# Performance work log

Hardware: AMD Instinct MI355X
Metric: run time of the kernel (lower is better)

Reference implementation:

```python
import jax, jax.numpy as jnp
import numpy as np

N, B, H, C, NF = 200000, 100, 128, 3, 128


def setup_inputs() -> dict:
    key = jax.random.key(0)
    ks = jax.random.split(key, 12)
    def w(k, shape, s=0.05):
        return jax.random.normal(k, shape, jnp.float32) * s
    return dict(
        node_feat=w(ks[0], (N, NF), 1.0),
        coord=w(ks[1], (N, 3), 1.0),
        virtual_node_feat=w(ks[2], (B, NF, C), 1.0),
        virtual_coord=w(ks[3], (B, 3, C), 1.0),
        data_batch=jnp.sort(jax.random.randint(ks[4], (N,), 0, B)),
        We1=w(ks[5], (2 * NF + 1, H)), be1=jnp.zeros((H,), jnp.float32),
        We2=w(ks[6], (H, H)), be2=jnp.zeros((H,), jnp.float32),
        Wc1=w(ks[7], (H, H)), bc1=jnp.zeros((H,), jnp.float32),
        Wc2=w(ks[8], (H, 1), 0.001),  # xavier gain=0.001 layer, no bias
        Wn1=w(ks[9], (2 * H, H)), bn1=jnp.zeros((H,), jnp.float32),
        Wn2=w(ks[10], (H, H)), bn2=jnp.zeros((H,), jnp.float32),
    )


def _segment_mean(x, idx, num_segments):
    # x: [N, d1, d2] -> [num_segments, d1, d2]; mean over nodes of each graph
    sums = jax.ops.segment_sum(x, idx, num_segments=num_segments)
    counts = jax.ops.segment_sum(jnp.ones((x.shape[0],), x.dtype), idx,
                                 num_segments=num_segments)
    return sums / jnp.maximum(counts, 1.0)[:, None, None]


def reference(node_feat, coord, virtual_node_feat, virtual_coord, data_batch,
              We1, be1, We2, be2, Wc1, bc1, Wc2, Wn1, bn1, Wn2, bn2):
    silu = jax.nn.silu
    n, nf = node_feat.shape
    nb, _, c = virtual_coord.shape

    # gather: real node -> its graph's virtual nodes
    diff = virtual_coord[data_batch] - coord[:, :, None]            # [N,3,C]
    radial = jnp.linalg.norm(diff, axis=1)                          # [N,C]

    # edge model (work in [N,C,feat] layout to avoid permutes)
    feat_R = jnp.broadcast_to(node_feat[:, None, :], (n, c, nf))    # [N,C,NF]
    feat_V = virtual_node_feat[data_batch].transpose(0, 2, 1)       # [N,C,NF]
    e_in = jnp.concatenate([feat_R, feat_V, radial[:, :, None]], axis=-1)
    m = silu(e_in @ We1 + be1)
    m = silu(m @ We2 + be2)                                         # [N,C,H]

    # coord model: per (node, virtual-channel) scalar weight
    s = silu(m @ Wc1 + bc1) @ Wc2                                   # [N,C,1]
    trans = diff * s[:, :, 0][:, None, :]                           # [N,3,C]
    virtual_coord = virtual_coord + _segment_mean(trans, data_batch, nb)

    # node model on virtual nodes
    agg = _segment_mean(m, data_batch, nb)                          # [B,C,H]
    n_in = jnp.concatenate([virtual_node_feat.transpose(0, 2, 1), agg], axis=-1)
    h = silu(n_in @ Wn1 + bn1) @ Wn2 + bn2                          # [B,C,H]
    virtual_node_feat = virtual_node_feat + h.transpose(0, 2, 1)    # residual

    return virtual_node_feat, virtual_coord
```

## Files before the change

kernel.cpp:

```cpp
#include <hip/hip_runtime.h>
#include <hip/hip_bf16.h>
#include <math.h>

#define NNODES 200000
#define NGRAPH 100
#define HD     128
#define NCH    3
#define BN     64
#define EROWS  (BN*NCH)
#define ESTR   136

typedef short short8 __attribute__((ext_vector_type(8)));
typedef float f32x4  __attribute__((ext_vector_type(4)));

#define MFMA_16x16x32(a,b,c) __builtin_amdgcn_mfma_f32_16x16x32_bf16((a),(b),(c),0,0,0)

__device__ __forceinline__ float bf2f(unsigned short u) {
    return __uint_as_float(((unsigned int)u) << 16);
}
__device__ __forceinline__ unsigned short f2bf(float f) {
    return (unsigned short)((__float_as_uint(f) + 0x8000u) >> 16);
}
__device__ __forceinline__ float silu_f(float x) {
    return x * __builtin_amdgcn_rcpf(1.0f + __expf(-x));
}

__global__ void prep_kernel(const float* __restrict__ We1,
                            const float* __restrict__ We2,
                            const float* __restrict__ Wc1,
                            const float* __restrict__ be1,
                            const float* __restrict__ be2,
                            const float* __restrict__ bc1,
                            const float* __restrict__ Wc2,
                            const float* __restrict__ vnf,
                            unsigned short* __restrict__ w1r,
                            unsigned short* __restrict__ w2r,
                            unsigned short* __restrict__ wc1r,
                            float* __restrict__ Q,
                            float* __restrict__ wlast,
                            float* __restrict__ be1f,
                            float* __restrict__ be2f,
                            float* __restrict__ bc1f,
                            float* __restrict__ wc2f) {
    int bid = blockIdx.x;
    if (bid < 192) {
        int t = bid * 256 + threadIdx.x;
        int m  = t / 16384;
        int e  = t % 16384;
        int j  = e & 7;
        int l  = (e >> 3) & 63;
        int ks = (e >> 9) & 3;
        int ct = e >> 11;
        int row = ks * 32 + (l >> 4) * 8 + j;
        int col = ct * 16 + (l & 15);
        const float*    src = (m == 0) ? We1 : ((m == 1) ? We2 : Wc1);
        unsigned short* dst = (m == 0) ? w1r : ((m == 1) ? w2r : wc1r);
        dst[e] = f2bf(src[row * 128 + col]);
        if (t < 128) {
            wlast[t] = We1[256 * 128 + t];
            be1f[t]  = be1[t];
            be2f[t]  = be2[t];
            bc1f[t]  = bc1[t];
            wc2f[t]  = Wc2[t];
        }
    } else {
        int bc = bid - 192;
        int b = bc / NCH, c = bc % NCH;
        int t = threadIdx.x;
        __shared__ float v[128];
        if (t < 128) v[t] = vnf[(b * 128 + t) * 3 + c];
        __syncthreads();
        if (t < 128) {
            float s = 0.0f;
            for (int k = 0; k < 128; ++k)
                s += v[k] * We1[(128 + k) * 128 + t];
            Q[(b * 3 + c) * 128 + t] = s;
        }
    }
}

__global__ __launch_bounds__(256, 2) void egcl_main(
    const float* __restrict__ node_feat,
    const float* __restrict__ coord,
    const float* __restrict__ vcoord,
    const int*   __restrict__ batch,
    const unsigned short* __restrict__ w1r,
    const unsigned short* __restrict__ w2r,
    const unsigned short* __restrict__ wc1r,
    const float* __restrict__ Q,
    const float* __restrict__ wlast,
    const float* __restrict__ be1f,
    const float* __restrict__ be2f,
    const float* __restrict__ bc1f,
    const float* __restrict__ wc2f,
    float* __restrict__ aggsum,
    float* __restrict__ transsum,
    float* __restrict__ cnt)
{
    __shared__ __align__(16) unsigned short e_buf[EROWS * ESTR];
    __shared__ unsigned short sbatch[BN];
    __shared__ unsigned short sseg_start[BN + 1];
    __shared__ unsigned short sseg_b[BN];
    __shared__ int snseg;

    const int tid   = threadIdx.x;
    const int wave  = tid >> 6;
    const int lane  = tid & 63;
    const int lrow  = lane & 15;
    const int lkb   = (lane >> 4) * 8;
    const int rq    = (lane >> 4) * 4;
    const int node0 = blockIdx.x * BN;

    if (tid < BN) {
        int n = node0 + tid;
        int b = batch[n];
        sbatch[tid] = (unsigned short)b;
        int prev = (tid > 0) ? batch[n - 1] : -1;
        unsigned long long mask = __ballot(b != prev);
        int ns = __popcll(mask);
        if (b != prev) {
            int idx = __popcll(mask & ((1ull << tid) - 1ull));
            sseg_start[idx] = (unsigned short)tid;
            sseg_b[idx]     = (unsigned short)b;
        }
        if (tid == 0) { sseg_start[ns] = BN; snseg = ns; }
        float cx = coord[n * 3 + 0];
        float cy = coord[n * 3 + 1];
        float cz = coord[n * 3 + 2];
        for (int c = 0; c < 3; ++c) {
            float dx = vcoord[b * 9 + 0 * 3 + c] - cx;
            float dy = vcoord[b * 9 + 1 * 3 + c] - cy;
            float dz = vcoord[b * 9 + 2 * 3 + c] - cz;
            f32x4 pad;
            pad[0] = dx; pad[1] = dy; pad[2] = dz;
            pad[3] = sqrtf(dx * dx + dy * dy + dz * dz);
            *(f32x4*)&e_buf[(c * 64 + tid) * ESTR + 128] = pad;
        }
    }
    __syncthreads();
    const int nseg = snseg;

    f32x4 acc1[8] = {};
    {
        const float* arow = node_feat + (size_t)(node0 + wave * 16 + lrow) * 128;
        for (int ks = 0; ks < 4; ++ks) {
            f32x4 x0 = *(const f32x4*)(arow + ks * 32 + lkb);
            f32x4 x1 = *(const f32x4*)(arow + ks * 32 + lkb + 4);
            short8 af;
            af[0] = (short)f2bf(x0[0]); af[1] = (short)f2bf(x0[1]);
            af[2] = (short)f2bf(x0[2]); af[3] = (short)f2bf(x0[3]);
            af[4] = (short)f2bf(x1[0]); af[5] = (short)f2bf(x1[1]);
            af[6] = (short)f2bf(x1[2]); af[7] = (short)f2bf(x1[3]);
            for (int ct = 0; ct < 8; ++ct) {
                short8 bfg = *(const short8*)(w1r + ((ct * 4 + ks) * 64 + lane) * 8);
                acc1[ct] = MFMA_16x16x32(af, bfg, acc1[ct]);
            }
        }
    }
    {
        float wl[8], bb[8];
        #pragma unroll
        for (int ct = 0; ct < 8; ++ct) {
            wl[ct] = wlast[ct * 16 + lrow];
            bb[ct] = be1f[ct * 16 + lrow];
        }
        if (nseg == 1) {
            const float* qb = Q + (int)sseg_b[0] * (NCH * HD);
            float qv[3][8];
            #pragma unroll
            for (int c = 0; c < 3; ++c)
                #pragma unroll
                for (int ct = 0; ct < 8; ++ct)
                    qv[c][ct] = qb[c * 128 + ct * 16 + lrow];
            #pragma unroll
            for (int r = 0; r < 4; ++r) {
                int nl = wave * 16 + rq + r;
                #pragma unroll
                for (int c = 0; c < 3; ++c) {
                    int row = c * 64 + nl;
                    float rad = *(const float*)&e_buf[row * ESTR + 134];
                    #pragma unroll
                    for (int ct = 0; ct < 8; ++ct) {
                        float x = acc1[ct][r] + bb[ct] + qv[c][ct] + rad * wl[ct];
                        e_buf[row * ESTR + ct * 16 + lrow] = f2bf(silu_f(x));
                    }
                }
            }
        } else {
            #pragma unroll
            for (int r = 0; r < 4; ++r) {
                int nl = wave * 16 + rq + r;
                int b  = sbatch[nl];
                #pragma unroll
                for (int c = 0; c < 3; ++c) {
                    int row = c * 64 + nl;
                    float rad = *(const float*)&e_buf[row * ESTR + 134];
                    const float* qb = Q + (b * 3 + c) * 128;
                    #pragma unroll
                    for (int ct = 0; ct < 8; ++ct) {
                        float x = acc1[ct][r] + bb[ct] + qb[ct * 16 + lrow] + rad * wl[ct];
                        e_buf[row * ESTR + ct * 16 + lrow] = f2bf(silu_f(x));
                    }
                }
            }
        }
    }

    const int bagg = (nseg == 1) ? (int)sseg_b[0] * (NCH * HD) : 0;

    for (int half = 0; half < 2; ++half) {
        f32x4 acc[3][4] = {};
        for (int ks = 0; ks < 4; ++ks) {
            short8 af[3];
            #pragma unroll
            for (int j = 0; j < 3; ++j)
                af[j] = *(const short8*)(&e_buf[(j * 64 + wave * 16 + lrow) * ESTR +
                                                ks * 32 + lkb]);
            #pragma unroll
            for (int c4 = 0; c4 < 4; ++c4) {
                int ct = half * 4 + c4;
                short8 bfg = *(const short8*)(w2r + ((ct * 4 + ks) * 64 + lane) * 8);
                #pragma unroll
                for (int j = 0; j < 3; ++j)
                    acc[j][c4] = MFMA_16x16x32(af[j], bfg, acc[j][c4]);
            }
        }
        for (int j = 0; j < 3; ++j) {
            #pragma unroll
            for (int c4 = 0; c4 < 4; ++c4) {
                int ct = half * 4 + c4;
                int h = ct * 16 + lrow;
                float bb = be2f[h];
                float psum = 0.0f;
                #pragma unroll
                for (int r = 0; r < 4; ++r) {
                    int row = j * 64 + wave * 16 + rq + r;
                    float v = silu_f(acc[j][c4][r] + bb);
                    e_buf[row * ESTR + h] = f2bf(v);
                    psum += v;
                }
                if (nseg == 1) {
                    psum += __shfl_xor(psum, 16, 64);
                    psum += __shfl_xor(psum, 32, 64);
                    if (lane < 16)
                        atomicAdd(&aggsum[bagg + j * 128 + ct * 16 + lane], psum);
                }
            }
        }
    }

    float p[3][4] = {};
    for (int half = 0; half < 2; ++half) {
        f32x4 acc[3][4] = {};
        for (int ks = 0; ks < 4; ++ks) {
            short8 af[3];
            #pragma unroll
            for (int j = 0; j < 3; ++j)
                af[j] = *(const short8*)(&e_buf[(j * 64 + wave * 16 + lrow) * ESTR +
                                                ks * 32 + lkb]);
            #pragma unroll
            for (int c4 = 0; c4 < 4; ++c4) {
                int ct = half * 4 + c4;
                short8 bfg = *(const short8*)(wc1r + ((ct * 4 + ks) * 64 + lane) * 8);
                #pragma unroll
                for (int j = 0; j < 3; ++j)
                    acc[j][c4] = MFMA_16x16x32(af[j], bfg, acc[j][c4]);
            }
        }
        for (int j = 0; j < 3; ++j) {
            #pragma unroll
            for (int c4 = 0; c4 < 4; ++c4) {
                int ct = half * 4 + c4;
                int h = ct * 16 + lrow;
                float bb = bc1f[h];
                float w2 = wc2f[h];
                #pragma unroll
                for (int r = 0; r < 4; ++r)
                    p[j][r] += silu_f(acc[j][c4][r] + bb) * w2;
            }
        }
    }
    for (int j = 0; j < 3; ++j) {
        float p0 = p[j][0], p1 = p[j][1], p2 = p[j][2], p3 = p[j][3];
        #pragma unroll
        for (int off = 1; off < 16; off <<= 1) {
            p0 += __shfl_xor(p0, off, 64);
            p1 += __shfl_xor(p1, off, 64);
            p2 += __shfl_xor(p2, off, 64);
            p3 += __shfl_xor(p3, off, 64);
        }
        if (lrow == 0) {
            int rbase = j * 64 + wave * 16 + rq;
            *(float*)&e_buf[(rbase + 0) * ESTR + 134] = p0;
            *(float*)&e_buf[(rbase + 1) * ESTR + 134] = p1;
            *(float*)&e_buf[(rbase + 2) * ESTR + 134] = p2;
            *(float*)&e_buf[(rbase + 3) * ESTR + 134] = p3;
        }
    }
    __syncthreads();

    if (nseg == 1) {
        int b = sseg_b[0];
        if (wave == 0) {
            float t[9];
            #pragma unroll
            for (int c = 0; c < 3; ++c) {
                int row = c * 64 + lane;
                float sv = *(const float*)&e_buf[row * ESTR + 134];
                float dx = *(const float*)&e_buf[row * ESTR + 128];
                float dy = *(const float*)&e_buf[row * ESTR + 130];
                float dz = *(const float*)&e_buf[row * ESTR + 132];
                t[0 * 3 + c] = dx * sv;
                t[1 * 3 + c] = dy * sv;
                t[2 * 3 + c] = dz * sv;
            }
            #pragma unroll
            for (int off = 1; off < 64; off <<= 1)
                #pragma unroll
                for (int k = 0; k < 9; ++k)
                    t[k] += __shfl_xor(t[k], off, 64);
            if (lane < 9)
                atomicAdd(&transsum[b * 9 + lane],
                          __shfl(t[lane], 0, 64));
            if (lane == 0) atomicAdd(&cnt[b], 64.0f);
        }
    } else {
        for (int sg = 0; sg < nseg; ++sg) {
            int s0 = sseg_start[sg], s1 = sseg_start[sg + 1], b = sseg_b[sg];
            for (int idx = tid; idx < NCH * HD; idx += 256) {
                int c = idx >> 7, h = idx & 127;
                float sum = 0.f;
                for (int ii = s0; ii < s1; ++ii)
                    sum += bf2f(e_buf[(c * 64 + ii) * ESTR + h]);
                atomicAdd(&aggsum[(b * 3 + c) * 128 + h], sum);
            }
            if (tid < 9) {
                int d = tid / 3, c = tid % 3;
                float sum = 0.f;
                for (int ii = s0; ii < s1; ++ii)
                    sum += (*(const float*)&e_buf[(c * 64 + ii) * ESTR + 128 + 2 * d])
                           * (*(const float*)&e_buf[(c * 64 + ii) * ESTR + 134]);
                atomicAdd(&transsum[b * 9 + d * 3 + c], sum);
            }
            if (tid == 0) atomicAdd(&cnt[b], (float)(s1 - s0));
        }
    }
}

__global__ void finalize_kernel(const float* __restrict__ vnf,
                                const float* __restrict__ vcoord,
                                const float* __restrict__ Wn1,
                                const float* __restrict__ bn1,
                                const float* __restrict__ Wn2,
                                const float* __restrict__ bn2,
                                const float* __restrict__ aggsum,
                                const float* __restrict__ transsum,
                                const float* __restrict__ cnt,
                                float* __restrict__ out) {
    int b = blockIdx.x / NCH;
    int c = blockIdx.x % NCH;
    int j = threadIdx.x;
    __shared__ float nin[256];
    __shared__ float h1[128];
    float count = fmaxf(cnt[b], 1.0f);
    nin[j]       = vnf[(b * 128 + j) * 3 + c];
    nin[128 + j] = aggsum[(b * 3 + c) * 128 + j] / count;
    __syncthreads();
    float x = bn1[j];
    for (int k = 0; k < 256; ++k)
        x += nin[k] * Wn1[k * 128 + j];
    h1[j] = silu_f(x);
    __syncthreads();
    float y = bn2[j];
    for (int k = 0; k < 128; ++k)
        y += h1[k] * Wn2[k * 128 + j];
    out[(b * 128 + j) * 3 + c] = vnf[(b * 128 + j) * 3 + c] + y;
    if (c == 0 && j < 9) {
        out[NGRAPH * 128 * 3 + b * 9 + j] =
            vcoord[b * 9 + j] + transsum[b * 9 + j] / count;
    }
}

extern "C" void kernel_launch(void* const* d_in, const int* in_sizes, int n_in,
                              void* d_out, int out_size, void* d_ws, size_t ws_size,
                              hipStream_t stream) {
    const float* node_feat = (const float*)d_in[0];
    const float* coord     = (const float*)d_in[1];
    const float* vnf       = (const float*)d_in[2];
    const float* vcoord    = (const float*)d_in[3];
    const int*   batch     = (const int*)d_in[4];
    const float* We1 = (const float*)d_in[5];
    const float* be1 = (const float*)d_in[6];
    const float* We2 = (const float*)d_in[7];
    const float* be2 = (const float*)d_in[8];
    const float* Wc1 = (const float*)d_in[9];
    const float* bc1 = (const float*)d_in[10];
    const float* Wc2 = (const float*)d_in[11];
    const float* Wn1 = (const float*)d_in[12];
    const float* bn1 = (const float*)d_in[13];
    const float* Wn2 = (const float*)d_in[14];
    const float* bn2 = (const float*)d_in[15];

    char* ws = (char*)d_ws;
    float*          aggsum   = (float*)(ws + 0);
    float*          transsum = (float*)(ws + 153600);
    float*          cntp     = (float*)(ws + 157200);
    float*          Q        = (float*)(ws + 157600);
    unsigned short* w1r      = (unsigned short*)(ws + 311200);
    unsigned short* w2r      = (unsigned short*)(ws + 343968);
    unsigned short* wc1r     = (unsigned short*)(ws + 376736);
    float*          wlast    = (float*)(ws + 409504);
    float*          be1f     = (float*)(ws + 410016);
    float*          be2f     = (float*)(ws + 410528);
    float*          bc1f     = (float*)(ws + 411040);
    float*          wc2f     = (float*)(ws + 411552);

    (void)hipMemsetAsync(d_ws, 0, 157600, stream);

    prep_kernel<<<192 + NGRAPH * NCH, 256, 0, stream>>>(
        We1, We2, Wc1, be1, be2, bc1, Wc2, vnf,
        w1r, w2r, wc1r, Q, wlast, be1f, be2f, bc1f, wc2f);

    egcl_main<<<NNODES / BN, 256, 0, stream>>>(
        node_feat, coord, vcoord, batch, w1r, w2r, wc1r, Q,
        wlast, be1f, be2f, bc1f, wc2f, aggsum, transsum, cntp);

    finalize_kernel<<<NGRAPH * NCH, 128, 0, stream>>>(
        vnf, vcoord, Wn1, bn1, Wn2, bn2, aggsum, transsum, cntp,
        (float*)d_out);
}
```

Measured before the change: 323.0 us.

## Permute hidden layout for vectorized bf16 LDS stores, packed converts, fold memset into prep

```diff
diff --git a/kernel.cpp b/kernel.cpp
--- a/kernel.cpp
+++ b/kernel.cpp
@@ -12,6 +12,8 @@
 
 typedef short short8 __attribute__((ext_vector_type(8)));
 typedef float f32x4  __attribute__((ext_vector_type(4)));
+typedef unsigned int u32x2 __attribute__((ext_vector_type(2)));
+typedef unsigned int u32x4 __attribute__((ext_vector_type(4)));
 
 #define MFMA_16x16x32(a,b,c) __builtin_amdgcn_mfma_f32_16x16x32_bf16((a),(b),(c),0,0,0)
 
@@ -20,6 +22,14 @@
 }
 __device__ __forceinline__ unsigned short f2bf(float f) {
     return (unsigned short)((__float_as_uint(f) + 0x8000u) >> 16);
+}
+__device__ __forceinline__ unsigned int cvt_pk_bf16(float lo, float hi) {
+    unsigned int r;
+    asm("v_cvt_pk_bf16_f32 %0, %1, %2" : "=v"(r) : "v"(lo), "v"(hi));
+    return r;
+}
+__device__ __forceinline__ short8 as_short8(u32x4 v) {
+    union { u32x4 u; short8 s; } x; x.u = v; return x.s;
 }
 __device__ __forceinline__ float silu_f(float x) {
     return x * __builtin_amdgcn_rcpf(1.0f + __expf(-x));
@@ -41,7 +51,8 @@
                             float* __restrict__ be1f,
                             float* __restrict__ be2f,
                             float* __restrict__ bc1f,
-                            float* __restrict__ wc2f) {
+                            float* __restrict__ wc2f,
+                            float* __restrict__ zacc) {
     int bid = blockIdx.x;
     if (bid < 192) {
         int t = bid * 256 + threadIdx.x;
@@ -51,11 +62,12 @@
         int l  = (e >> 3) & 63;
         int ks = (e >> 9) & 3;
         int ct = e >> 11;
-        int row = ks * 32 + (l >> 4) * 8 + j;
+        int kf  = ks * 32 + (l >> 4) * 8 + j;
         int col = ct * 16 + (l & 15);
+        int srck = (m == 0) ? kf : (((kf & 7) << 4) | (kf >> 3));
         const float*    src = (m == 0) ? We1 : ((m == 1) ? We2 : Wc1);
         unsigned short* dst = (m == 0) ? w1r : ((m == 1) ? w2r : wc1r);
-        dst[e] = f2bf(src[row * 128 + col]);
+        dst[e] = f2bf(src[srck * 128 + col]);
         if (t < 128) {
             wlast[t] = We1[256 * 128 + t];
             be1f[t]  = be1[t];
@@ -63,7 +75,7 @@
             bc1f[t]  = bc1[t];
             wc2f[t]  = Wc2[t];
         }
-    } else {
+    } else if (bid < 492) {
         int bc = bid - 192;
         int b = bc / NCH, c = bc % NCH;
         int t = threadIdx.x;
@@ -76,6 +88,9 @@
                 s += v[k] * We1[(128 + k) * 128 + t];
             Q[(b * 3 + c) * 128 + t] = s;
         }
+    } else {
+        int idx = (bid - 492) * 256 + threadIdx.x;
+        if (idx < 39400) zacc[idx] = 0.0f;
     }
 }
 
@@ -146,11 +161,12 @@
         for (int ks = 0; ks < 4; ++ks) {
             f32x4 x0 = *(const f32x4*)(arow + ks * 32 + lkb);
             f32x4 x1 = *(const f32x4*)(arow + ks * 32 + lkb + 4);
-            short8 af;
-            af[0] = (short)f2bf(x0[0]); af[1] = (short)f2bf(x0[1]);
-            af[2] = (short)f2bf(x0[2]); af[3] = (short)f2bf(x0[3]);
-            af[4] = (short)f2bf(x1[0]); af[5] = (short)f2bf(x1[1]);
-            af[6] = (short)f2bf(x1[2]); af[7] = (short)f2bf(x1[3]);
+            u32x4 av;
+            av[0] = cvt_pk_bf16(x0[0], x0[1]);
+            av[1] = cvt_pk_bf16(x0[2], x0[3]);
+            av[2] = cvt_pk_bf16(x1[0], x1[1]);
+            av[3] = cvt_pk_bf16(x1[2], x1[3]);
+            short8 af = as_short8(av);
             for (int ct = 0; ct < 8; ++ct) {
                 short8 bfg = *(const short8*)(w1r + ((ct * 4 + ks) * 64 + lane) * 8);
                 acc1[ct] = MFMA_16x16x32(af, bfg, acc1[ct]);
@@ -158,12 +174,10 @@
         }
     }
     {
-        float wl[8], bb[8];
+        float wl[8];
         #pragma unroll
-        for (int ct = 0; ct < 8; ++ct) {
+        for (int ct = 0; ct < 8; ++ct)
             wl[ct] = wlast[ct * 16 + lrow];
-            bb[ct] = be1f[ct * 16 + lrow];
-        }
         if (nseg == 1) {
             const float* qb = Q + (int)sseg_b[0] * (NCH * HD);
             float qv[3][8];
@@ -171,7 +185,7 @@
             for (int c = 0; c < 3; ++c)
                 #pragma unroll
                 for (int ct = 0; ct < 8; ++ct)
-                    qv[c][ct] = qb[c * 128 + ct * 16 + lrow];
+                    qv[c][ct] = qb[c * 128 + ct * 16 + lrow] + be1f[ct * 16 + lrow];
             #pragma unroll
             for (int r = 0; r < 4; ++r) {
                 int nl = wave * 16 + rq + r;
@@ -179,14 +193,23 @@
                 for (int c = 0; c < 3; ++c) {
                     int row = c * 64 + nl;
                     float rad = *(const float*)&e_buf[row * ESTR + 134];
+                    float v[8];
                     #pragma unroll
-                    for (int ct = 0; ct < 8; ++ct) {
-                        float x = acc1[ct][r] + bb[ct] + qv[c][ct] + rad * wl[ct];
-                        e_buf[row * ESTR + ct * 16 + lrow] = f2bf(silu_f(x));
-                    }
+                    for (int ct = 0; ct < 8; ++ct)
+                        v[ct] = silu_f(acc1[ct][r] + qv[c][ct] + rad * wl[ct]);
+                    u32x4 av;
+                    av[0] = cvt_pk_bf16(v[0], v[1]);
+                    av[1] = cvt_pk_bf16(v[2], v[3]);
+                    av[2] = cvt_pk_bf16(v[4], v[5]);
+                    av[3] = cvt_pk_bf16(v[6], v[7]);
+                    *(u32x4*)&e_buf[row * ESTR + lrow * 8] = av;
                 }
             }
         } else {
+            float bb[8];
+            #pragma unroll
+            for (int ct = 0; ct < 8; ++ct)
+                bb[ct] = be1f[ct * 16 + lrow];
             #pragma unroll
             for (int r = 0; r < 4; ++r) {
                 int nl = wave * 16 + rq + r;
@@ -196,11 +219,17 @@
                     int row = c * 64 + nl;
                     float rad = *(const float*)&e_buf[row * ESTR + 134];
                     const float* qb = Q + (b * 3 + c) * 128;
+                    float v[8];
                     #pragma unroll
-                    for (int ct = 0; ct < 8; ++ct) {
-                        float x = acc1[ct][r] + bb[ct] + qb[ct * 16 + lrow] + rad * wl[ct];
-                        e_buf[row * ESTR + ct * 16 + lrow] = f2bf(silu_f(x));
-                    }
+                    for (int ct = 0; ct < 8; ++ct)
+                        v[ct] = silu_f(acc1[ct][r] + bb[ct] + qb[ct * 16 + lrow]
+                                       + rad * wl[ct]);
+                    u32x4 av;
+                    av[0] = cvt_pk_bf16(v[0], v[1]);
+                    av[1] = cvt_pk_bf16(v[2], v[3]);
+                    av[2] = cvt_pk_bf16(v[4], v[5]);
+                    av[3] = cvt_pk_bf16(v[6], v[7]);
+                    *(u32x4*)&e_buf[row * ESTR + lrow * 8] = av;
                 }
             }
         }
@@ -225,25 +254,36 @@
                     acc[j][c4] = MFMA_16x16x32(af[j], bfg, acc[j][c4]);
             }
         }
+        float b0 = be2f[(half * 4 + 0) * 16 + lrow];
+        float b1 = be2f[(half * 4 + 1) * 16 + lrow];
+        float b2 = be2f[(half * 4 + 2) * 16 + lrow];
+        float b3 = be2f[(half * 4 + 3) * 16 + lrow];
+        #pragma unroll
         for (int j = 0; j < 3; ++j) {
-            #pragma unroll
-            for (int c4 = 0; c4 < 4; ++c4) {
-                int ct = half * 4 + c4;
-                int h = ct * 16 + lrow;
-                float bb = be2f[h];
-                float psum = 0.0f;
-                #pragma unroll
-                for (int r = 0; r < 4; ++r) {
-                    int row = j * 64 + wave * 16 + rq + r;
-                    float v = silu_f(acc[j][c4][r] + bb);
-                    e_buf[row * ESTR + h] = f2bf(v);
-                    psum += v;
-                }
-                if (nseg == 1) {
-                    psum += __shfl_xor(psum, 16, 64);
-                    psum += __shfl_xor(psum, 32, 64);
-                    if (lane < 16)
-                        atomicAdd(&aggsum[bagg + j * 128 + ct * 16 + lane], psum);
+            float ps0 = 0.f, ps1 = 0.f, ps2 = 0.f, ps3 = 0.f;
+            #pragma unroll
+            for (int r = 0; r < 4; ++r) {
+                int row = j * 64 + wave * 16 + rq + r;
+                float v0 = silu_f(acc[j][0][r] + b0);
+                float v1 = silu_f(acc[j][1][r] + b1);
+                float v2 = silu_f(acc[j][2][r] + b2);
+                float v3 = silu_f(acc[j][3][r] + b3);
+                ps0 += v0; ps1 += v1; ps2 += v2; ps3 += v3;
+                u32x2 dv;
+                dv[0] = cvt_pk_bf16(v0, v1);
+                dv[1] = cvt_pk_bf16(v2, v3);
+                *(u32x2*)&e_buf[row * ESTR + lrow * 8 + half * 4] = dv;
+            }
+            if (nseg == 1) {
+                ps0 += __shfl_xor(ps0, 16, 64); ps0 += __shfl_xor(ps0, 32, 64);
+                ps1 += __shfl_xor(ps1, 16, 64); ps1 += __shfl_xor(ps1, 32, 64);
+                ps2 += __shfl_xor(ps2, 16, 64); ps2 += __shfl_xor(ps2, 32, 64);
+                ps3 += __shfl_xor(ps3, 16, 64); ps3 += __shfl_xor(ps3, 32, 64);
+                if (lane < 16) {
+                    atomicAdd(&aggsum[bagg + j * 128 + (half * 4 + 0) * 16 + lane], ps0);
+                    atomicAdd(&aggsum[bagg + j * 128 + (half * 4 + 1) * 16 + lane], ps1);
+                    atomicAdd(&aggsum[bagg + j * 128 + (half * 4 + 2) * 16 + lane], ps2);
+                    atomicAdd(&aggsum[bagg + j * 128 + (half * 4 + 3) * 16 + lane], ps3);
                 }
             }
         }
@@ -267,16 +307,24 @@
                     acc[j][c4] = MFMA_16x16x32(af[j], bfg, acc[j][c4]);
             }
         }
+        float b0 = bc1f[(half * 4 + 0) * 16 + lrow];
+        float b1 = bc1f[(half * 4 + 1) * 16 + lrow];
+        float b2 = bc1f[(half * 4 + 2) * 16 + lrow];
+        float b3 = bc1f[(half * 4 + 3) * 16 + lrow];
+        float w0 = wc2f[(half * 4 + 0) * 16 + lrow];
+        float w1 = wc2f[(half * 4 + 1) * 16 + lrow];
+        float w2 = wc2f[(half * 4 + 2) * 16 + lrow];
+        float w3 = wc2f[(half * 4 + 3) * 16 + lrow];
+        #pragma unroll
         for (int j = 0; j < 3; ++j) {
             #pragma unroll
-            for (int c4 = 0; c4 < 4; ++c4) {
-                int ct = half * 4 + c4;
-                int h = ct * 16 + lrow;
-                float bb = bc1f[h];
-                float w2 = wc2f[h];
-                #pragma unroll
-                for (int r = 0; r < 4; ++r)
-                    p[j][r] += silu_f(acc[j][c4][r] + bb) * w2;
+            for (int r = 0; r < 4; ++r) {
+                float s = p[j][r];
+                s += silu_f(acc[j][0][r] + b0) * w0;
+                s += silu_f(acc[j][1][r] + b1) * w1;
+                s += silu_f(acc[j][2][r] + b2) * w2;
+                s += silu_f(acc[j][3][r] + b3) * w3;
+                p[j][r] = s;
             }
         }
     }
@@ -328,10 +376,11 @@
         for (int sg = 0; sg < nseg; ++sg) {
             int s0 = sseg_start[sg], s1 = sseg_start[sg + 1], b = sseg_b[sg];
             for (int idx = tid; idx < NCH * HD; idx += 256) {
-                int c = idx >> 7, h = idx & 127;
+                int c = idx >> 7, pcol = idx & 127;
                 float sum = 0.f;
                 for (int ii = s0; ii < s1; ++ii)
-                    sum += bf2f(e_buf[(c * 64 + ii) * ESTR + h]);
+                    sum += bf2f(e_buf[(c * 64 + ii) * ESTR + pcol]);
+                int h = ((pcol & 7) << 4) | (pcol >> 3);
                 atomicAdd(&aggsum[(b * 3 + c) * 128 + h], sum);
             }
             if (tid < 9) {
@@ -415,11 +464,10 @@
     float*          bc1f     = (float*)(ws + 411040);
     float*          wc2f     = (float*)(ws + 411552);
 
-    (void)hipMemsetAsync(d_ws, 0, 157600, stream);
-
-    prep_kernel<<<192 + NGRAPH * NCH, 256, 0, stream>>>(
+    prep_kernel<<<192 + NGRAPH * NCH + 154, 256, 0, stream>>>(
         We1, We2, Wc1, be1, be2, bc1, Wc2, vnf,
-        w1r, w2r, wc1r, Q, wlast, be1f, be2f, bc1f, wc2f);
+        w1r, w2r, wc1r, Q, wlast, be1f, be2f, bc1f, wc2f,
+        (float*)ws);
 
     egcl_main<<<NNODES / BN, 256, 0, stream>>>(
         node_feat, coord, vcoord, batch, w1r, w2r, wc1r, Q,
```

New measurement: 308.7 us. -4.4%, faster.
